# Optimization experiments

Measured on AMD Instinct MI355X. Metric: run time of the kernel, lower is better.

Reference implementation:

```python
import jax, jax.numpy as jnp
import numpy as np

B, S, D = 8, 2048, 1024


def setup_inputs() -> dict:
    key = jax.random.key(0)
    k1, k2, k3, k4, k5 = jax.random.split(key, 5)
    scale = 1.0 / np.sqrt(D)
    x = jax.random.normal(k1, (B, S, D), dtype=jnp.float32)
    Wq = jax.random.normal(k2, (D, D), dtype=jnp.float32) * scale
    Wk = jax.random.normal(k3, (D, D), dtype=jnp.float32) * scale
    Wv = jax.random.normal(k4, (D, D), dtype=jnp.float32) * scale
    # sequence lengths in [1, S]
    lens = jax.random.randint(k5, (B,), 1, S + 1, dtype=jnp.int32)
    return {"x": x, "lens": lens, "Wq": Wq, "Wk": Wk, "Wv": Wv}


def reference(x, lens, Wq, Wk, Wv):
    # nn.Linear(bias=False): y = x @ W.T
    q = jnp.einsum('bsd,ed->bse', x, Wq)
    k = jnp.einsum('bsd,ed->bse', x, Wk)
    v = jnp.einsum('bsd,ed->bse', x, Wv)
    # scores: QK^T / sqrt(D)  -> [B, S, S]
    scores = jnp.einsum('bqd,bkd->bqk', q, k) / jnp.sqrt(jnp.asarray(D, x.dtype))
    # key-padding mask from lens: True where key position >= len (masked to -inf)
    key_pad = jnp.arange(S)[None, :] >= lens[:, None]          # [B, S]
    scores = jnp.where(key_pad[:, None, :], -jnp.inf, scores)  # broadcast over query dim
    att = jax.nn.softmax(scores, axis=2)
    return jnp.einsum('bqk,bkd->bqd', att, v)
```

## Files before the change

### kernel.cpp

```cpp
#include <hip/hip_runtime.h>
#include <stdint.h>

typedef __bf16 bf16;
typedef __bf16 bf16x8 __attribute__((ext_vector_type(8)));
typedef __bf16 bf16x4 __attribute__((ext_vector_type(4)));
typedef float f32x4 __attribute__((ext_vector_type(4)));
typedef float f32x16 __attribute__((ext_vector_type(16)));

#define DEV static __device__ __forceinline__

DEV void async_copy16(const bf16* gsrc, const bf16* ldst) {
  __builtin_amdgcn_global_load_lds(
      (__attribute__((address_space(1))) void*)(uintptr_t)gsrc,
      (__attribute__((address_space(3))) void*)(uint32_t)(uintptr_t)ldst,
      16, 0, 0);
}

DEV void gemm_tile16(const bf16* __restrict__ A, const bf16* __restrict__ B,
                     int lda, int ldb, int kTiles,
                     bf16* As, bf16* Bs, f32x4 acc[4][4]) {
  const int tid  = threadIdx.x;
  const int wave = tid >> 6;
  const int lane = tid & 63;
  const int wm = (wave >> 1) * 64;
  const int wn = (wave & 1) * 64;
  const int mf = lane & 15;
  const int jb = lane >> 4;
  const int sw = (mf & 7) * 8;

  const int srow = tid >> 3;
  const int scol = ((tid & 7) ^ (srow & 7)) * 8;
  const bf16* Ag = A + (size_t)srow * lda + scol;
  const bf16* Bg = B + (size_t)srow * ldb + scol;
  bf16* Asw = As + wave * 512;
  bf16* Bsw = Bs + wave * 512;

  for (int kt = 0; kt < kTiles; ++kt) {
    __syncthreads();
    const bf16* ag = Ag + kt * 64;
    const bf16* bg = Bg + kt * 64;
#pragma unroll
    for (int i = 0; i < 4; ++i) {
      async_copy16(ag + (size_t)(i * 32) * lda, Asw + i * 2048);
      async_copy16(bg + (size_t)(i * 32) * ldb, Bsw + i * 2048);
    }
    __syncthreads();
#pragma unroll
    for (int ks = 0; ks < 2; ++ks) {
      const int j8 = (ks * 4 + jb) * 8;
      bf16x8 af[4], bv[4];
#pragma unroll
      for (int i = 0; i < 4; ++i)
        af[i] = *(const bf16x8*)&As[(wm + i * 16 + mf) * 64 + (j8 ^ sw)];
#pragma unroll
      for (int j = 0; j < 4; ++j)
        bv[j] = *(const bf16x8*)&Bs[(wn + j * 16 + mf) * 64 + (j8 ^ sw)];
#pragma unroll
      for (int i = 0; i < 4; ++i)
#pragma unroll
        for (int j = 0; j < 4; ++j)
          acc[i][j] = __builtin_amdgcn_mfma_f32_16x16x32_bf16(af[i], bv[j], acc[i][j], 0, 0, 0);
    }
  }
}

DEV void gemm_tile32(const bf16* __restrict__ A, const bf16* __restrict__ B,
                     int lda, int ldb, int kTiles,
                     bf16* As, bf16* Bs, f32x16 acc[2][2]) {
  const int tid  = threadIdx.x;
  const int wave = tid >> 6;
  const int lane = tid & 63;
  const int wm = (wave >> 1) * 64;
  const int wn = (wave & 1) * 64;
  const int rf = lane & 31;
  const int kh = (lane >> 5) * 8;
  const int sw = (lane & 7) * 8;

  const int srow = tid >> 3;
  const int scol = ((tid & 7) ^ (srow & 7)) * 8;
  const bf16* Ag = A + (size_t)srow * lda + scol;
  const bf16* Bg = B + (size_t)srow * ldb + scol;
  bf16* Asw = As + wave * 512;
  bf16* Bsw = Bs + wave * 512;

  for (int kt = 0; kt < kTiles; ++kt) {
    __syncthreads();
    const bf16* ag = Ag + kt * 64;
    const bf16* bg = Bg + kt * 64;
#pragma unroll
    for (int i = 0; i < 4; ++i) {
      async_copy16(ag + (size_t)(i * 32) * lda, Asw + i * 2048);
      async_copy16(bg + (size_t)(i * 32) * ldb, Bsw + i * 2048);
    }
    __syncthreads();
#pragma unroll
    for (int ks = 0; ks < 4; ++ks) {
      const int off = (ks * 16 + kh) ^ sw;
      bf16x8 a0 = *(const bf16x8*)&As[(wm + rf) * 64 + off];
      bf16x8 a1 = *(const bf16x8*)&As[(wm + 32 + rf) * 64 + off];
      bf16x8 b0 = *(const bf16x8*)&Bs[(wn + rf) * 64 + off];
      bf16x8 b1 = *(const bf16x8*)&Bs[(wn + 32 + rf) * 64 + off];
      acc[0][0] = __builtin_amdgcn_mfma_f32_32x32x16_bf16(a0, b0, acc[0][0], 0, 0, 0);
      acc[0][1] = __builtin_amdgcn_mfma_f32_32x32x16_bf16(a0, b1, acc[0][1], 0, 0, 0);
      acc[1][0] = __builtin_amdgcn_mfma_f32_32x32x16_bf16(a1, b0, acc[1][0], 0, 0, 0);
      acc[1][1] = __builtin_amdgcn_mfma_f32_32x32x16_bf16(a1, b1, acc[1][1], 0, 0, 0);
    }
  }
}

#define EPILOGUE16(STMT)                                                     \
  do {                                                                       \
    const int lane = threadIdx.x & 63, wave = threadIdx.x >> 6;              \
    const int colb = n0 + (wave & 1) * 64 + (lane & 15);                     \
    const int rowb = m0 + (wave >> 1) * 64 + (lane >> 4) * 4;                \
    _Pragma("unroll") for (int i = 0; i < 4; ++i)                            \
      _Pragma("unroll") for (int r = 0; r < 4; ++r) {                        \
        size_t row = rowb + i * 16 + r;                                      \
        _Pragma("unroll") for (int j = 0; j < 4; ++j) {                      \
          size_t col = colb + j * 16;                                        \
          float val = acc[i][j][r];                                          \
          STMT;                                                              \
        }                                                                    \
      }                                                                      \
  } while (0)

#define EPILOGUE32(STMT)                                                     \
  do {                                                                       \
    const int lane = threadIdx.x & 63, wave = threadIdx.x >> 6;              \
    const int colb = n0 + (wave & 1) * 64 + (lane & 31);                     \
    const int rowb = m0 + (wave >> 1) * 64 + (lane >> 5) * 4;                \
    _Pragma("unroll") for (int i = 0; i < 2; ++i)                            \
      _Pragma("unroll") for (int reg = 0; reg < 16; ++reg) {                 \
        size_t row = rowb + i * 32 + (reg & 3) + 8 * (reg >> 2);             \
        _Pragma("unroll") for (int j = 0; j < 2; ++j) {                      \
          size_t col = colb + j * 32;                                        \
          float val = acc[i][j][reg];                                        \
          STMT;                                                              \
        }                                                                    \
      }                                                                      \
  } while (0)

__global__ __launch_bounds__(256) void k_cast_all(const float* __restrict__ X,
                                                  const float* __restrict__ Wq,
                                                  const float* __restrict__ Wk,
                                                  const float* __restrict__ Wv,
                                                  bf16* __restrict__ Xb,
                                                  bf16* __restrict__ Wb) {
  int i = blockIdx.x * 256 + threadIdx.x;
  const float* src;
  bf16* dst;
  int off;
  if (i < 4194304) {
    src = X; dst = Xb; off = i;
  } else {
    int j = i - 4194304;
    int which = j >> 18;
    src = (which == 0) ? Wq : ((which == 1) ? Wk : Wv);
    dst = Wb + (size_t)(j >> 18) * 1048576;
    off = j & 262143;
  }
  float4 v = ((const float4*)src)[off];
  bf16x4 o = {(bf16)v.x, (bf16)v.y, (bf16)v.z, (bf16)v.w};
  ((bf16x4*)dst)[off] = o;
}

__global__ __launch_bounds__(256) void k_gemm_qkv(const bf16* __restrict__ X,
                                                  const bf16* __restrict__ W,
                                                  const int* __restrict__ lens,
                                                  bf16* __restrict__ QKV,
                                                  bf16* __restrict__ Vt) {
  const int n0 = blockIdx.x * 128;
  const int m0 = blockIdx.y * 128;
  if (n0 >= 1024 && (m0 & 2047) >= lens[m0 >> 11]) return;
  __shared__ __align__(16) bf16 sbuf[128 * 128];
  bf16* As = sbuf;
  bf16* Bs = sbuf + 128 * 64;
  f32x4 acc[4][4] = {};
  gemm_tile16(X + (size_t)m0 * 1024, W + (size_t)n0 * 1024, 1024, 1024, 16, As, Bs, acc);

  if (n0 < 2048) {
    const float qscale = (n0 < 1024) ? 0.03125f : 1.0f;
    EPILOGUE16(QKV[row * 3072 + col] = (bf16)(val * qscale));
  } else {
    __syncthreads();
    const int lane = threadIdx.x & 63, wave = threadIdx.x >> 6;
    const int dl0 = (wave & 1) * 64 + (lane & 15);
    const int sl0 = (wave >> 1) * 64 + ((lane >> 4) << 2);
#pragma unroll
    for (int i = 0; i < 4; ++i) {
      const int s = sl0 + i * 16;
      const int h = s >> 3, lo = s & 7;
#pragma unroll
      for (int j = 0; j < 4; ++j) {
        const int d = dl0 + j * 16;
        bf16x4 o = {(bf16)acc[i][j][0], (bf16)acc[i][j][1],
                    (bf16)acc[i][j][2], (bf16)acc[i][j][3]};
        *(bf16x4*)&sbuf[d * 128 + ((h ^ (d & 15)) << 3) + lo] = o;
      }
    }
    __syncthreads();
    const int q = lane >> 4, p = lane & 15;
    bf16* Vb = Vt + ((size_t)(m0 >> 11) * 1024 + (n0 - 2048)) * 2048 + (m0 & 2047);
#pragma unroll
    for (int it = 0; it < 8; ++it) {
      const int d = wave * 32 + it * 4 + q;
      bf16x8 v = *(const bf16x8*)&sbuf[d * 128 + ((p ^ (d & 15)) << 3)];
      *(bf16x8*)&Vb[(size_t)d * 2048 + p * 8] = v;
    }
  }
}

__global__ __launch_bounds__(256) void k_gemm_scores(const bf16* __restrict__ QKV,
                                                     const int* __restrict__ lens,
                                                     bf16* __restrict__ S) {
  const int b = blockIdx.z;
  const int len = lens[b];
  const int n0 = blockIdx.x * 128;
  if (n0 >= len) return;
  const int m0 = blockIdx.y * 128;
  __shared__ __align__(16) bf16 As[128 * 64];
  __shared__ __align__(16) bf16 Bs[128 * 64];
  const bf16* Q = QKV + (size_t)b * 2048 * 3072;
  const bf16* K = Q + 1024;
  f32x16 acc[2][2] = {};
  gemm_tile32(Q + (size_t)m0 * 3072, K + (size_t)n0 * 3072, 3072, 3072, 16, As, Bs, acc);
  bf16* Sb = S + (size_t)b * 2048 * 2048;
  EPILOGUE32(Sb[row * 2048 + col] = (bf16)val);
}

__global__ __launch_bounds__(256) void k_softmax(bf16* __restrict__ S,
                                                 const int* __restrict__ lens) {
  const int row = blockIdx.x;
  const int len = lens[row >> 11];
  const int kmax = (len + 63) & ~63;
  bf16* Sr = S + (size_t)row * 2048;
  const int tid = threadIdx.x;
  const int base = tid * 8;
  __shared__ float red[4];

  float f[8];
  if (base < len) {
    bf16x8 v = ((const bf16x8*)Sr)[tid];
#pragma unroll
    for (int e = 0; e < 8; ++e) f[e] = (base + e < len) ? (float)v[e] : -1e30f;
  } else {
#pragma unroll
    for (int e = 0; e < 8; ++e) f[e] = -1e30f;
  }
  float m = -1e30f;
#pragma unroll
  for (int e = 0; e < 8; ++e) m = fmaxf(m, f[e]);
#pragma unroll
  for (int off = 32; off; off >>= 1) m = fmaxf(m, __shfl_xor(m, off));
  if ((tid & 63) == 0) red[tid >> 6] = m;
  __syncthreads();
  m = fmaxf(fmaxf(red[0], red[1]), fmaxf(red[2], red[3]));
  __syncthreads();

  float s = 0.f;
#pragma unroll
  for (int e = 0; e < 8; ++e) {
    float p = (base + e < len) ? __expf(f[e] - m) : 0.f;
    f[e] = p;
    s += p;
  }
#pragma unroll
  for (int off = 32; off; off >>= 1) s += __shfl_xor(s, off);
  if ((tid & 63) == 0) red[tid >> 6] = s;
  __syncthreads();
  s = red[0] + red[1] + red[2] + red[3];
  const float inv = 1.f / s;

  if (base < kmax) {
    bf16x8 o;
#pragma unroll
    for (int e = 0; e < 8; ++e) o[e] = (bf16)(f[e] * inv);
    ((bf16x8*)Sr)[tid] = o;
  }
}

__global__ __launch_bounds__(256) void k_gemm_out(const bf16* __restrict__ P,
                                                  const bf16* __restrict__ Vt,
                                                  const int* __restrict__ lens,
                                                  float* __restrict__ Out) {
  const int b = blockIdx.z;
  const int kTiles = (lens[b] + 63) >> 6;
  const int n0 = blockIdx.x * 128;
  const int m0 = blockIdx.y * 128;
  __shared__ __align__(16) bf16 As[128 * 64];
  __shared__ __align__(16) bf16 Bs[128 * 64];
  const bf16* Pb = P + (size_t)b * 2048 * 2048;
  const bf16* Vb = Vt + (size_t)b * 1024 * 2048;
  f32x16 acc[2][2] = {};
  gemm_tile32(Pb + (size_t)m0 * 2048, Vb + (size_t)n0 * 2048, 2048, 2048, kTiles, As, Bs, acc);
  float* Ob = Out + (size_t)b * 2048 * 1024;
  EPILOGUE32(Ob[row * 1024 + col] = val);
}

extern "C" void kernel_launch(void* const* d_in, const int* in_sizes, int n_in,
                              void* d_out, int out_size, void* d_ws, size_t ws_size,
                              hipStream_t stream) {
  const float* x   = (const float*)d_in[0];
  const int* lens  = (const int*)d_in[1];
  const float* Wq  = (const float*)d_in[2];
  const float* Wk  = (const float*)d_in[3];
  const float* Wv  = (const float*)d_in[4];
  float* out = (float*)d_out;

  char* ws = (char*)d_ws;
  bf16* S   = (bf16*)(ws);
  bf16* Xb  = (bf16*)(ws);
  bf16* Wb  = (bf16*)(ws + 33554432);
  bf16* QKV = (bf16*)(ws + 67108864);
  bf16* Vt  = (bf16*)(ws + 167772160);

  k_cast_all<<<19456, 256, 0, stream>>>(x, Wq, Wk, Wv, Xb, Wb);
  k_gemm_qkv<<<dim3(24, 128), 256, 0, stream>>>(Xb, Wb, lens, QKV, Vt);
  k_gemm_scores<<<dim3(16, 16, 8), 256, 0, stream>>>(QKV, lens, S);
  k_softmax<<<16384, 256, 0, stream>>>(S, lens);
  k_gemm_out<<<dim3(8, 16, 8), 256, 0, stream>>>(S, Vt, lens, out);
}
```

Before: 353.0 us.

## Fuse softmax normalization into PV GEMM A-tile load, store only row stats

The softmax kernel now only computes each row's max and inverse sum and writes them as a float2 per row, instead of rewriting the normalized probability matrix. The output GEMM loads raw scores through registers, applies exp and scaling while filling shared memory, and keeps the async copy only for the V tiles. This removes one full write pass over the scores matrix and its later reread as probabilities. In exchange, the exp work is repeated for every output column tile (8x), and the A operand now goes through a synchronous register path instead of direct async copies. The stats buffer reuses the QKV workspace region, which is only safe if QKV is no longer needed when k_stats writes to it.

```diff
diff --git a/kernel.cpp b/kernel.cpp
--- a/kernel.cpp
+++ b/kernel.cpp
@@ -91,6 +91,67 @@
     for (int i = 0; i < 4; ++i) {
       async_copy16(ag + (size_t)(i * 32) * lda, Asw + i * 2048);
       async_copy16(bg + (size_t)(i * 32) * ldb, Bsw + i * 2048);
+    }
+    __syncthreads();
+#pragma unroll
+    for (int ks = 0; ks < 4; ++ks) {
+      const int off = (ks * 16 + kh) ^ sw;
+      bf16x8 a0 = *(const bf16x8*)&As[(wm + rf) * 64 + off];
+      bf16x8 a1 = *(const bf16x8*)&As[(wm + 32 + rf) * 64 + off];
+      bf16x8 b0 = *(const bf16x8*)&Bs[(wn + rf) * 64 + off];
+      bf16x8 b1 = *(const bf16x8*)&Bs[(wn + 32 + rf) * 64 + off];
+      acc[0][0] = __builtin_amdgcn_mfma_f32_32x32x16_bf16(a0, b0, acc[0][0], 0, 0, 0);
+      acc[0][1] = __builtin_amdgcn_mfma_f32_32x32x16_bf16(a0, b1, acc[0][1], 0, 0, 0);
+      acc[1][0] = __builtin_amdgcn_mfma_f32_32x32x16_bf16(a1, b0, acc[1][0], 0, 0, 0);
+      acc[1][1] = __builtin_amdgcn_mfma_f32_32x32x16_bf16(a1, b1, acc[1][1], 0, 0, 0);
+    }
+  }
+}
+
+DEV void gemm_tile32_expA(const bf16* __restrict__ A, const bf16* __restrict__ B,
+                          int lda, int ldb, int kTiles, int len,
+                          const float2* __restrict__ statsRow,
+                          bf16* As, bf16* Bs, f32x16 acc[2][2]) {
+  const int tid  = threadIdx.x;
+  const int wave = tid >> 6;
+  const int lane = tid & 63;
+  const int wm = (wave >> 1) * 64;
+  const int wn = (wave & 1) * 64;
+  const int rf = lane & 31;
+  const int kh = (lane >> 5) * 8;
+  const int sw = (lane & 7) * 8;
+
+  const int srow = tid >> 3;
+  const int scol = ((tid & 7) ^ (srow & 7)) * 8;
+  const bf16* Ag = A + (size_t)srow * lda + scol;
+  const bf16* Bg = B + (size_t)srow * ldb + scol;
+  bf16* Bsw = Bs + wave * 512;
+
+  float mrow[4], irow[4];
+#pragma unroll
+  for (int i = 0; i < 4; ++i) {
+    float2 st = statsRow[srow + i * 32];
+    mrow[i] = st.x;
+    irow[i] = st.y;
+  }
+
+  for (int kt = 0; kt < kTiles; ++kt) {
+    __syncthreads();
+    const bf16* bg = Bg + kt * 64;
+#pragma unroll
+    for (int i = 0; i < 4; ++i)
+      async_copy16(bg + (size_t)(i * 32) * ldb, Bsw + i * 2048);
+    const int colbase = kt * 64 + scol;
+#pragma unroll
+    for (int i = 0; i < 4; ++i) {
+      bf16x8 s8 = *(const bf16x8*)(Ag + (size_t)(i * 32) * lda + kt * 64);
+      bf16x8 o;
+#pragma unroll
+      for (int e = 0; e < 8; ++e) {
+        float p = (colbase + e < len) ? __expf((float)s8[e] - mrow[i]) * irow[i] : 0.f;
+        o[e] = (bf16)p;
+      }
+      *(bf16x8*)&As[wave * 512 + i * 2048 + lane * 8] = o;
     }
     __syncthreads();
 #pragma unroll
@@ -228,12 +289,12 @@
   EPILOGUE32(Sb[row * 2048 + col] = (bf16)val);
 }
 
-__global__ __launch_bounds__(256) void k_softmax(bf16* __restrict__ S,
-                                                 const int* __restrict__ lens) {
+__global__ __launch_bounds__(256) void k_stats(const bf16* __restrict__ S,
+                                               const int* __restrict__ lens,
+                                               float2* __restrict__ stats) {
   const int row = blockIdx.x;
   const int len = lens[row >> 11];
-  const int kmax = (len + 63) & ~63;
-  bf16* Sr = S + (size_t)row * 2048;
+  const bf16* Sr = S + (size_t)row * 2048;
   const int tid = threadIdx.x;
   const int base = tid * 8;
   __shared__ float red[4];
@@ -259,40 +320,35 @@
 
   float s = 0.f;
 #pragma unroll
-  for (int e = 0; e < 8; ++e) {
-    float p = (base + e < len) ? __expf(f[e] - m) : 0.f;
-    f[e] = p;
-    s += p;
-  }
+  for (int e = 0; e < 8; ++e)
+    if (base + e < len) s += __expf(f[e] - m);
 #pragma unroll
   for (int off = 32; off; off >>= 1) s += __shfl_xor(s, off);
   if ((tid & 63) == 0) red[tid >> 6] = s;
   __syncthreads();
-  s = red[0] + red[1] + red[2] + red[3];
-  const float inv = 1.f / s;
-
-  if (base < kmax) {
-    bf16x8 o;
-#pragma unroll
-    for (int e = 0; e < 8; ++e) o[e] = (bf16)(f[e] * inv);
-    ((bf16x8*)Sr)[tid] = o;
-  }
-}
-
-__global__ __launch_bounds__(256) void k_gemm_out(const bf16* __restrict__ P,
+  if (tid == 0) {
+    s = red[0] + red[1] + red[2] + red[3];
+    stats[row] = make_float2(m, 1.f / s);
+  }
+}
+
+__global__ __launch_bounds__(256) void k_gemm_out(const bf16* __restrict__ S,
                                                   const bf16* __restrict__ Vt,
                                                   const int* __restrict__ lens,
+                                                  const float2* __restrict__ stats,
                                                   float* __restrict__ Out) {
   const int b = blockIdx.z;
-  const int kTiles = (lens[b] + 63) >> 6;
+  const int len = lens[b];
+  const int kTiles = (len + 63) >> 6;
   const int n0 = blockIdx.x * 128;
   const int m0 = blockIdx.y * 128;
   __shared__ __align__(16) bf16 As[128 * 64];
   __shared__ __align__(16) bf16 Bs[128 * 64];
-  const bf16* Pb = P + (size_t)b * 2048 * 2048;
+  const bf16* Sb = S + (size_t)b * 2048 * 2048;
   const bf16* Vb = Vt + (size_t)b * 1024 * 2048;
   f32x16 acc[2][2] = {};
-  gemm_tile32(Pb + (size_t)m0 * 2048, Vb + (size_t)n0 * 2048, 2048, 2048, kTiles, As, Bs, acc);
+  gemm_tile32_expA(Sb + (size_t)m0 * 2048, Vb + (size_t)n0 * 2048, 2048, 2048,
+                   kTiles, len, stats + (size_t)b * 2048 + m0, As, Bs, acc);
   float* Ob = Out + (size_t)b * 2048 * 1024;
   EPILOGUE32(Ob[row * 1024 + col] = val);
 }
@@ -308,15 +364,16 @@
   float* out = (float*)d_out;
 
   char* ws = (char*)d_ws;
-  bf16* S   = (bf16*)(ws);
-  bf16* Xb  = (bf16*)(ws);
-  bf16* Wb  = (bf16*)(ws + 33554432);
-  bf16* QKV = (bf16*)(ws + 67108864);
-  bf16* Vt  = (bf16*)(ws + 167772160);
+  bf16* S     = (bf16*)(ws);
+  bf16* Xb    = (bf16*)(ws);
+  bf16* Wb    = (bf16*)(ws + 33554432);
+  bf16* QKV   = (bf16*)(ws + 67108864);
+  float2* stats = (float2*)(ws + 67108864);
+  bf16* Vt    = (bf16*)(ws + 167772160);
 
   k_cast_all<<<19456, 256, 0, stream>>>(x, Wq, Wk, Wv, Xb, Wb);
   k_gemm_qkv<<<dim3(24, 128), 256, 0, stream>>>(Xb, Wb, lens, QKV, Vt);
   k_gemm_scores<<<dim3(16, 16, 8), 256, 0, stream>>>(QKV, lens, S);
-  k_softmax<<<16384, 256, 0, stream>>>(S, lens);
-  k_gemm_out<<<dim3(8, 16, 8), 256, 0, stream>>>(S, Vt, lens, out);
-}
+  k_stats<<<16384, 256, 0, stream>>>(S, lens, stats);
+  k_gemm_out<<<dim3(8, 16, 8), 256, 0, stream>>>(S, Vt, lens, stats, out);
+}
```

After: 367.8 us. +4.2%, slower.
